# Performance work log

Hardware: AMD Instinct MI355X
Metric: run time of the kernel (lower is better)

The kernel has to match this reference:

```python
import jax, jax.numpy as jnp
import numpy as np

MAX_VISIT = 200
NUM_CODE = 506          # feature vocab -> 507 multi-hot dims
NUM_TGT = 284           # target vocab multi-hot dims
B = 64
P = 40                  # codes per visit
D_OTH = 57              # others feature dim (sign slice [37:] is 20-dim)
K = 100                 # len(weight_idx)
LSTM = 256
D_FEAT = (NUM_CODE + 1) + K + 27 + (D_OTH - 37)   # 654
D_FWD = D_FEAT + 10                                # 664
D_MLP_IN = (NUM_CODE + 1) + (D_OTH - 37) + 20 + 8  # 555


def multi_hot(codes, n):
    """Binary multi-hot encode int codes over last axis. codes: [..., P]."""
    shp = codes.shape
    flat = codes.reshape(-1, shp[-1])
    R = flat.shape[0]
    rows = jnp.repeat(jnp.arange(R), shp[-1])
    z = jnp.zeros((R, n), jnp.float32).at[rows, flat.reshape(-1)].set(1.0)
    return z.reshape(shp[:-1] + (n,))


def reverse_sequence(x, lengths):
    """tf.reverse_sequence along axis 1: reverse first lengths[i] steps, keep rest."""
    T = x.shape[1]
    j = jnp.arange(T)[None, :]
    L = lengths[:, None]
    idx = jnp.where(j < L, L - 1 - j, j)          # [B, T]
    return jnp.take_along_axis(x, idx[:, :, None], axis=1)


def setup_inputs() -> dict:
    key = jax.random.key(0)
    ks = jax.random.split(key, 13)
    code = jax.random.randint(ks[0], (B, MAX_VISIT, P), 0, NUM_CODE + 1, dtype=jnp.int32)
    others = jax.random.normal(ks[1], (B, MAX_VISIT, D_OTH), jnp.float32)
    length = jax.random.randint(ks[2], (B,), 3, MAX_VISIT + 1, dtype=jnp.int32)
    target = jax.random.randint(ks[3], (B, 10), 0, NUM_TGT, dtype=jnp.int32)
    weight_idx = jax.random.randint(ks[4], (K,), 0, NUM_TGT, dtype=jnp.int32)
    s = 0.02
    Wf = jax.random.normal(ks[5], (D_FWD, LSTM), jnp.float32) * s
    bf = jnp.zeros((LSTM,), jnp.float32)
    Wb = jax.random.normal(ks[6], (D_FWD, LSTM), jnp.float32) * s
    bb = jnp.zeros((LSTM,), jnp.float32)
    W0 = jax.random.normal(ks[7], (D_MLP_IN, 256), jnp.float32) * s
    b0 = jnp.zeros((256,), jnp.float32)
    W1 = jax.random.normal(ks[8], (256, 256), jnp.float32) * s
    b1 = jnp.zeros((256,), jnp.float32)
    return {"code": code, "others": others, "length": length, "target": target,
            "weight_idx": weight_idx, "Wf": Wf, "bf": bf, "Wb": Wb, "bb": bb,
            "W0": W0, "b0": b0, "W1": W1, "b1": b1}


def reference(code, others, length, target, weight_idx, Wf, bf, Wb, bb, W0, b0, W1, b1):
    code_mh = multi_hot(code, NUM_CODE + 1)                      # [B,200,507]
    # valid-visit mask (dense analogue of tf.boolean_mask over [B,198])
    mask = (jnp.arange(MAX_VISIT - 2)[None, :] < (length - 2)[:, None]).astype(jnp.float32)
    sign = others[:, 1:-1, 37:]                                  # [B,198,20]
    interval_ = jnp.concatenate([others[:, 1:-1, 27:37], others[:, 2:, 27:37]], axis=-1)
    stay = others[:, 1:-1, 19:27]
    x = jnp.concatenate([code_mh[:, 1:-1], sign, interval_, stay], axis=-1)  # [B,198,555]
    h = jax.nn.relu(x @ W0 + b0) @ W1 + b1                       # [B,198,256]
    fv = h / jnp.sqrt(jnp.sum(h * h, axis=-1, keepdims=True))
    fv = fv * mask[:, :, None]                                   # zero invalid rows
    # target block: gather (1 - multi-hot) at weight_idx, tile over visits
    tgt = 1.0 - multi_hot(target, NUM_TGT)                       # [B,284]
    tgt = tgt[:, weight_idx]                                     # [B,K]
    tgt = jnp.broadcast_to(tgt[:, None, :], (B, MAX_VISIT, K))
    code_full = jnp.concatenate([code_mh, tgt], axis=-1)         # [B,200,607]
    interval = others[:, :, 27:37]
    interval_backward = jnp.concatenate(
        [jnp.zeros((B, 1, 10), jnp.float32), reverse_sequence(interval, length)[:, :-1]], axis=1)
    feature = jnp.concatenate([code_full, others[:, :, :27], others[:, :, 37:]], axis=-1)
    feature_backward = reverse_sequence(feature, length)
    x_forward = jnp.concatenate([feature, interval], axis=-1)[:, :-2] @ Wf + bf
    x_backward = jnp.concatenate([feature_backward, interval_backward], axis=-1)[:, :-2] @ Wb + bb
    return (x_forward, x_backward, fv)
```

## Files before the change

### kernel.cpp

```cpp
#include <hip/hip_runtime.h>
#include <hip/hip_bf16.h>

typedef unsigned short u16;
typedef __attribute__((ext_vector_type(8))) short short8;
typedef __attribute__((ext_vector_type(4))) float f32x4;

#define TMAX 200
#define TOUT 198
#define PC 40
#define DOTH 57
#define NKT 9
#define FWD_OFF 0
#define BWD_OFF 3244032
#define FV_OFF  6488064
#define OWF 0
#define OWB 294912
#define OW0 589824
#define OW1 884736
#define OTF 1015808
#define OTB 1081344

__device__ __forceinline__ u16 f2b(float v) {
  __hip_bfloat16 h = __float2bfloat16(v);
  return *(u16*)&h;
}

__global__ __launch_bounds__(256) void prep_kernel(
    const int* __restrict__ target, const int* __restrict__ widx,
    const float* __restrict__ Wf, const float* __restrict__ bfv,
    const float* __restrict__ Wb, const float* __restrict__ bbv,
    const float* __restrict__ W0, const float* __restrict__ W1,
    u16* __restrict__ wsu, float* __restrict__ wsf)
{
  int blk = blockIdx.x, n = threadIdx.x;
  if (blk < 248) {
    const float* src; u16* dst; int kb; int mode;
    if (blk < 72)       { src=Wf; dst=wsu+OWF/2; kb=blk;     mode=0; }
    else if (blk < 144) { src=Wb; dst=wsu+OWB/2; kb=blk-72;  mode=0; }
    else if (blk < 216) { src=W0; dst=wsu+OW0/2; kb=blk-144; mode=1; }
    else                { src=W1; dst=wsu+OW1/2; kb=blk-216; mode=2; }
    u16 pk[8];
    #pragma unroll
    for (int j=0;j<8;j++) {
      int k = kb*8+j;
      int sr;
      if (mode==0)      sr = (k<57)? 607+k : (k<564)? k-57 : -1;
      else if (mode==1) sr = (k<48)? 507+k : (k<57)? -1 : (k<564)? k-57 : -1;
      else              sr = k;
      float v = (sr>=0)? src[sr*256+n] : 0.f;
      pk[j] = f2b(v);
    }
    *(uint4*)(dst + (kb*256+n)*8) = *(uint4*)pk;
  } else {
    int b = blk - 248;
    __shared__ float tval[100]; __shared__ int tg[10];
    if (n<10) tg[n]=target[b*10+n];
    __syncthreads();
    if (n<100){ int w=widx[n]; float v=1.f;
      #pragma unroll
      for(int i=0;i<10;i++) if(tg[i]==w) v=0.f;
      tval[n]=v; }
    __syncthreads();
    float aF=bfv[n], aB=bbv[n];
    for(int k=0;k<100;k++){ float v=tval[k];
      aF=fmaf(v,Wf[(507+k)*256+n],aF); aB=fmaf(v,Wb[(507+k)*256+n],aB); }
    wsf[OTF/4 + b*256+n]=aF; wsf[OTB/4 + b*256+n]=aB;
  }
}

__global__ __launch_bounds__(256) void gemm_kernel(
    const int* __restrict__ code, const float* __restrict__ others,
    const int* __restrict__ length,
    const float* __restrict__ b0, const float* __restrict__ b1,
    const u16* __restrict__ wsu, const float* __restrict__ wsf,
    float* __restrict__ out)
{
  const int tile = blockIdx.x;
  const int strm = blockIdx.y;
  const int tid = threadIdx.x;
  const int wv = tid>>6, lane = tid&63, q = lane>>4, c = lane&15;
  const int colbase = wv*64 + c;

  __shared__ u16 lA[3][2048];
  __shared__ int rowB[32], rowT[32], rowS[32], rowS2[32], rowL[32];
  __shared__ float rpart[4][32];

  if (tid < 32) {
    int m = tile*32 + tid;
    int b = m/198, t = m - b*198;
    int L = length[b];
    int s, s2 = 0;
    if (strm==0) s = t;
    else if (strm==1){ s = (t<L)? (L-1-t) : t;
                       s2 = (t==0)? -1 : (((t-1)<L)? (L-t) : (t-1)); }
    else s = t+1;
    rowB[tid]=b; rowT[tid]=t; rowS[tid]=s; rowS2[tid]=s2; rowL[tid]=L;
  }
  __syncthreads();

  int myp[5], myr[5];
  #pragma unroll
  for (int it=0; it<5; it++) {
    int idx = tid + it*256;
    int r = idx/40, p = idx - r*40;
    myr[it] = r*8;
    myp[it] = 57 + code[(rowB[r]*TMAX + rowS[r])*PC + p];
  }

  float dv[8];
  if (strm < 2) {
    #pragma unroll
    for (int it=0; it<8; it++) {
      int idx = tid + it*256;
      float v = 0.f;
      if (idx < 32*57) {
        int r = idx/57, j = idx - r*57;
        int col = (j<27)? j : (j<47)? 37+(j-27) : 27+(j-47);
        int sr = (strm==1 && j>=47)? rowS2[r] : rowS[r];
        if (sr >= 0) v = others[(rowB[r]*TMAX + sr)*DOTH + col];
      }
      dv[it] = v;
    }
  } else {
    #pragma unroll
    for (int it=0; it<6; it++) {
      int idx = tid + it*256;
      int r = idx/48, j = idx - r*48;
      int t = rowT[r], srow, col;
      if (j<20)      { srow=t+1; col=37+j; }
      else if (j<30) { srow=t+1; col=27+(j-20); }
      else if (j<40) { srow=t+2; col=27+(j-30); }
      else           { srow=t+1; col=19+(j-40); }
      dv[it] = others[(rowB[r]*TMAX + srow)*DOTH + col];
    }
  }

  f32x4 acc[2][4];
  if (strm < 2) {
    const float* tg = wsf + ((strm==0)? OTF/4 : OTB/4);
    #pragma unroll
    for (int mt=0; mt<2; mt++)
      #pragma unroll
      for (int reg=0; reg<4; reg++) {
        int rl = mt*16 + q*4 + reg;
        const float* tr = tg + rowB[rl]*256;
        #pragma unroll
        for (int nt=0; nt<4; nt++) acc[mt][nt][reg] = tr[colbase + nt*16];
      }
  } else {
    #pragma unroll
    for (int nt=0; nt<4; nt++){ float v = b0[colbase + nt*16];
      #pragma unroll
      for (int mt=0; mt<2; mt++)
        #pragma unroll
        for (int reg=0; reg<4; reg++) acc[mt][nt][reg]=v; }
  }

  { uint4 z = {0,0,0,0};
    ((uint4*)lA[0])[tid] = z; ((uint4*)lA[1])[tid] = z; }
  __syncthreads();
  #pragma unroll
  for (int it=0; it<5; it++) {
    unsigned d = (unsigned)(myp[it]);
    if (d < 64u) lA[0][(d>>3)*256 + myr[it] + (d&7)] = 0x3F80;
  }
  if (strm < 2) {
    #pragma unroll
    for (int it=0; it<8; it++) {
      int idx = tid + it*256;
      if (idx < 32*57) {
        int r = idx/57, j = idx - r*57;
        lA[0][(j>>3)*256 + r*8 + (j&7)] = f2b(dv[it]);
      }
    }
  } else {
    #pragma unroll
    for (int it=0; it<6; it++) {
      int idx = tid + it*256;
      int r = idx/48, j = idx - r*48;
      lA[0][(j>>3)*256 + r*8 + (j&7)] = f2b(dv[it]);
    }
  }
  __syncthreads();

  const u16* Wpk = wsu + ((strm==0)? OWF/2 : (strm==1)? OWB/2 : OW0/2);
  for (int kt=0; kt<NKT; kt++) {
    const u16* A = lA[kt%3];
    const u16* gB0 = Wpk + ((kt*8 + q    )*256 + colbase)*8;
    const u16* gB1 = Wpk + ((kt*8 + 4 + q)*256 + colbase)*8;
    short8 bf0[4], bf1[4];
    #pragma unroll
    for (int nt=0; nt<4; nt++) bf0[nt] = *(const short8*)(gB0 + nt*16*8);
    #pragma unroll
    for (int nt=0; nt<4; nt++) bf1[nt] = *(const short8*)(gB1 + nt*16*8);
    if (kt < 8) {
      u16* nb = lA[(kt+1)%3];
      const int k0n = (kt+1)*64;
      #pragma unroll
      for (int it=0; it<5; it++) {
        unsigned d = (unsigned)(myp[it] - k0n);
        if (d < 64u) nb[(d>>3)*256 + myr[it] + (d&7)] = 0x3F80;
      }
    }
    if (kt < 7) {
      uint4 z = {0,0,0,0};
      ((uint4*)lA[(kt+2)%3])[tid] = z;
    }
    short8 af0[2], af1[2];
    #pragma unroll
    for (int mt=0; mt<2; mt++) af0[mt] = *(const short8*)&A[(q    )*256 + (mt*16 + c)*8];
    #pragma unroll
    for (int mt=0; mt<2; mt++) af1[mt] = *(const short8*)&A[(4 + q)*256 + (mt*16 + c)*8];
    #pragma unroll
    for (int mt=0; mt<2; mt++)
      #pragma unroll
      for (int nt=0; nt<4; nt++)
        acc[mt][nt] = __builtin_amdgcn_mfma_f32_16x16x32_bf16(af0[mt], bf0[nt], acc[mt][nt], 0,0,0);
    #pragma unroll
    for (int mt=0; mt<2; mt++)
      #pragma unroll
      for (int nt=0; nt<4; nt++)
        acc[mt][nt] = __builtin_amdgcn_mfma_f32_16x16x32_bf16(af1[mt], bf1[nt], acc[mt][nt], 0,0,0);
    __syncthreads();
  }

  if (strm < 2) {
    float* o = out + ((strm==0)? FWD_OFF : BWD_OFF);
    #pragma unroll
    for (int mt=0; mt<2; mt++)
      #pragma unroll
      for (int reg=0; reg<4; reg++) {
        int rl = mt*16 + q*4 + reg;
        float* orow = o + (rowB[rl]*TOUT + rowT[rl])*256 + colbase;
        #pragma unroll
        for (int nt=0; nt<4; nt++) orow[nt*16] = acc[mt][nt][reg];
      }
  } else {
    if (wv == 0) {
      #pragma unroll
      for (int mt=0; mt<2; mt++)
        #pragma unroll
        for (int reg=0; reg<4; reg++) {
          int rl = mt*16 + q*4 + reg;
          #pragma unroll
          for (int nt=0; nt<4; nt++) {
            int kl = c + nt*16;
            lA[0][(kl>>3)*256 + rl*8 + (kl&7)] = f2b(fmaxf(acc[mt][nt][reg], 0.f));
          }
        }
    }
    __syncthreads();
    f32x4 a2[2][4];
    #pragma unroll
    for (int nt=0; nt<4; nt++){ float v = b1[colbase + nt*16];
      #pragma unroll
      for (int mt=0; mt<2; mt++)
        #pragma unroll
        for (int reg=0; reg<4; reg++) a2[mt][nt][reg]=v; }
    const u16* W1p = wsu + OW1/2;
    for (int kt2=0; kt2<4; kt2++) {
      if (wv == kt2+1) {
        u16* B2 = lA[(kt2+1)&1];
        #pragma unroll
        for (int mt=0; mt<2; mt++)
          #pragma unroll
          for (int reg=0; reg<4; reg++) {
            int rl = mt*16 + q*4 + reg;
            #pragma unroll
            for (int nt=0; nt<4; nt++) {
              int kl = c + nt*16;
              B2[(kl>>3)*256 + rl*8 + (kl&7)] = f2b(fmaxf(acc[mt][nt][reg], 0.f));
            }
          }
      }
      const u16* A2 = lA[kt2&1];
      #pragma unroll
      for (int s=0; s<2; s++) {
        int akb = s*4 + q;
        const u16* gB = W1p + ((kt2*8 + akb)*256 + colbase)*8;
        short8 af[2], bf[4];
        #pragma unroll
        for (int nt=0; nt<4; nt++) bf[nt] = *(const short8*)(gB + nt*16*8);
        #pragma unroll
        for (int mt=0; mt<2; mt++) af[mt] = *(const short8*)&A2[akb*256 + (mt*16 + c)*8];
        #pragma unroll
        for (int mt=0; mt<2; mt++)
          #pragma unroll
          for (int nt=0; nt<4; nt++)
            a2[mt][nt] = __builtin_amdgcn_mfma_f32_16x16x32_bf16(af[mt], bf[nt], a2[mt][nt], 0,0,0);
      }
      __syncthreads();
    }
    #pragma unroll
    for (int mt=0; mt<2; mt++)
      #pragma unroll
      for (int reg=0; reg<4; reg++) {
        int rl = mt*16 + q*4 + reg;
        float ss = 0.f;
        #pragma unroll
        for (int nt=0; nt<4; nt++){ float v=a2[mt][nt][reg]; ss = fmaf(v,v,ss); }
        ss += __shfl_xor(ss, 1, 64); ss += __shfl_xor(ss, 2, 64);
        ss += __shfl_xor(ss, 4, 64); ss += __shfl_xor(ss, 8, 64);
        if (c==0) rpart[wv][rl] = ss;
      }
    __syncthreads();
    #pragma unroll
    for (int mt=0; mt<2; mt++)
      #pragma unroll
      for (int reg=0; reg<4; reg++) {
        int rl = mt*16 + q*4 + reg;
        float s = rpart[0][rl]+rpart[1][rl]+rpart[2][rl]+rpart[3][rl];
        float inv = (s>0.f)? (1.0f/sqrtf(s)) : 0.f;
        int t = rowT[rl];
        if (t >= rowL[rl]-2) inv = 0.f;
        float* orow = out + FV_OFF + (rowB[rl]*TOUT + t)*256 + colbase;
        #pragma unroll
        for (int nt=0; nt<4; nt++) orow[nt*16] = a2[mt][nt][reg]*inv;
      }
  }
}

extern "C" void kernel_launch(void* const* d_in, const int* in_sizes, int n_in,
                              void* d_out, int out_size, void* d_ws, size_t ws_size,
                              hipStream_t stream) {
  const int*   code    = (const int*)d_in[0];
  const float* others  = (const float*)d_in[1];
  const int*   length  = (const int*)d_in[2];
  const int*   target  = (const int*)d_in[3];
  const int*   widx    = (const int*)d_in[4];
  const float* Wf      = (const float*)d_in[5];
  const float* bfv     = (const float*)d_in[6];
  const float* Wb      = (const float*)d_in[7];
  const float* bbv     = (const float*)d_in[8];
  const float* W0      = (const float*)d_in[9];
  const float* b0v     = (const float*)d_in[10];
  const float* W1      = (const float*)d_in[11];
  const float* b1v     = (const float*)d_in[12];

  u16*   wsu = (u16*)d_ws;
  float* wsf = (float*)d_ws;
  float* out = (float*)d_out;

  prep_kernel<<<dim3(312), dim3(256), 0, stream>>>(target, widx, Wf, bfv, Wb, bbv, W0, W1, wsu, wsf);
  gemm_kernel<<<dim3(396,3), dim3(256), 0, stream>>>(code, others, length,
      b0v, b1v, wsu, wsf, out);
}
```

Before: 122.3 us.

## Prefetch weight tiles one step ahead and skip fully masked MLP tiles

The GEMM k-loops now double-buffer the B-operand (weight) fragments in registers, so the next k-step's global loads are issued before the current MFMAs run, and both loops are fully unrolled. In the MLP stream, a tile whose rows all fall beyond the valid length (masked to zero in the output) now writes zeros and exits early instead of computing the MLP. This hides global weight-load latency and avoids wasted work, at the cost of more registers, which could reduce occupancy.

After: 121.4 us. No clear change (-0.7%).

```diff
diff --git a/kernel.cpp b/kernel.cpp
--- a/kernel.cpp
+++ b/kernel.cpp
@@ -84,7 +84,9 @@
   __shared__ u16 lA[3][2048];
   __shared__ int rowB[32], rowT[32], rowS[32], rowS2[32], rowL[32];
   __shared__ float rpart[4][32];
-
+  __shared__ int s_skip;
+
+  if (tid == 0) s_skip = 1;
   if (tid < 32) {
     int m = tile*32 + tid;
     int b = m/198, t = m - b*198;
@@ -98,6 +100,21 @@
   }
   __syncthreads();
 
+  if (strm == 2) {
+    if (tid < 32 && rowT[tid] < rowL[tid]-2) s_skip = 0;
+    __syncthreads();
+    if (s_skip) {
+      f32x4 z = {0.f, 0.f, 0.f, 0.f};
+      #pragma unroll
+      for (int it=0; it<8; it++) {
+        int lin = it*256 + tid;
+        int r = lin>>6, c4 = (lin&63)<<2;
+        *(f32x4*)(out + FV_OFF + (rowB[r]*TOUT + rowT[r])*256 + c4) = z;
+      }
+      return;
+    }
+  }
+
   int myp[5], myr[5];
   #pragma unroll
   for (int it=0; it<5; it++) {
@@ -156,6 +173,18 @@
         for (int reg=0; reg<4; reg++) acc[mt][nt][reg]=v; }
   }
 
+  const u16* Wpk = wsu + ((strm==0)? OWF/2 : (strm==1)? OWB/2 : OW0/2);
+  short8 bb[2][8];
+  {
+    const u16* gB0 = Wpk + ((q    )*256 + colbase)*8;
+    const u16* gB1 = Wpk + ((4 + q)*256 + colbase)*8;
+    #pragma unroll
+    for (int nt=0; nt<4; nt++) {
+      bb[0][nt]   = *(const short8*)(gB0 + nt*128);
+      bb[0][nt+4] = *(const short8*)(gB1 + nt*128);
+    }
+  }
+
   { uint4 z = {0,0,0,0};
     ((uint4*)lA[0])[tid] = z; ((uint4*)lA[1])[tid] = z; }
   __syncthreads();
@@ -183,17 +212,24 @@
   }
   __syncthreads();
 
-  const u16* Wpk = wsu + ((strm==0)? OWF/2 : (strm==1)? OWB/2 : OW0/2);
+  #pragma unroll
   for (int kt=0; kt<NKT; kt++) {
     const u16* A = lA[kt%3];
-    const u16* gB0 = Wpk + ((kt*8 + q    )*256 + colbase)*8;
-    const u16* gB1 = Wpk + ((kt*8 + 4 + q)*256 + colbase)*8;
-    short8 bf0[4], bf1[4];
-    #pragma unroll
-    for (int nt=0; nt<4; nt++) bf0[nt] = *(const short8*)(gB0 + nt*16*8);
-    #pragma unroll
-    for (int nt=0; nt<4; nt++) bf1[nt] = *(const short8*)(gB1 + nt*16*8);
-    if (kt < 8) {
+    short8 af0[2], af1[2];
+    #pragma unroll
+    for (int mt=0; mt<2; mt++) af0[mt] = *(const short8*)&A[(q    )*256 + (mt*16 + c)*8];
+    #pragma unroll
+    for (int mt=0; mt<2; mt++) af1[mt] = *(const short8*)&A[(4 + q)*256 + (mt*16 + c)*8];
+    if (kt < NKT-1) {
+      const u16* gB0 = Wpk + (((kt+1)*8 + q    )*256 + colbase)*8;
+      const u16* gB1 = Wpk + (((kt+1)*8 + 4 + q)*256 + colbase)*8;
+      #pragma unroll
+      for (int nt=0; nt<4; nt++) {
+        bb[(kt+1)&1][nt]   = *(const short8*)(gB0 + nt*128);
+        bb[(kt+1)&1][nt+4] = *(const short8*)(gB1 + nt*128);
+      }
+    }
+    if (kt < NKT-1) {
       u16* nb = lA[(kt+1)%3];
       const int k0n = (kt+1)*64;
       #pragma unroll
@@ -202,25 +238,20 @@
         if (d < 64u) nb[(d>>3)*256 + myr[it] + (d&7)] = 0x3F80;
       }
     }
-    if (kt < 7) {
+    if (kt < NKT-2) {
       uint4 z = {0,0,0,0};
       ((uint4*)lA[(kt+2)%3])[tid] = z;
     }
-    short8 af0[2], af1[2];
-    #pragma unroll
-    for (int mt=0; mt<2; mt++) af0[mt] = *(const short8*)&A[(q    )*256 + (mt*16 + c)*8];
-    #pragma unroll
-    for (int mt=0; mt<2; mt++) af1[mt] = *(const short8*)&A[(4 + q)*256 + (mt*16 + c)*8];
     #pragma unroll
     for (int mt=0; mt<2; mt++)
       #pragma unroll
       for (int nt=0; nt<4; nt++)
-        acc[mt][nt] = __builtin_amdgcn_mfma_f32_16x16x32_bf16(af0[mt], bf0[nt], acc[mt][nt], 0,0,0);
+        acc[mt][nt] = __builtin_amdgcn_mfma_f32_16x16x32_bf16(af0[mt], bb[kt&1][nt], acc[mt][nt], 0,0,0);
     #pragma unroll
     for (int mt=0; mt<2; mt++)
       #pragma unroll
       for (int nt=0; nt<4; nt++)
-        acc[mt][nt] = __builtin_amdgcn_mfma_f32_16x16x32_bf16(af1[mt], bf1[nt], acc[mt][nt], 0,0,0);
+        acc[mt][nt] = __builtin_amdgcn_mfma_f32_16x16x32_bf16(af1[mt], bb[kt&1][nt+4], acc[mt][nt], 0,0,0);
     __syncthreads();
   }
 
@@ -249,6 +280,13 @@
           }
         }
     }
+    const u16* W1p = wsu + OW1/2;
+    short8 bw[2][4];
+    {
+      const u16* gB = W1p + ((q)*256 + colbase)*8;
+      #pragma unroll
+      for (int nt=0; nt<4; nt++) bw[0][nt] = *(const short8*)(gB + nt*128);
+    }
     __syncthreads();
     f32x4 a2[2][4];
     #pragma unroll
@@ -257,7 +295,7 @@
       for (int mt=0; mt<2; mt++)
         #pragma unroll
         for (int reg=0; reg<4; reg++) a2[mt][nt][reg]=v; }
-    const u16* W1p = wsu + OW1/2;
+    #pragma unroll
     for (int kt2=0; kt2<4; kt2++) {
       if (wv == kt2+1) {
         u16* B2 = lA[(kt2+1)&1];
@@ -273,21 +311,25 @@
             }
           }
       }
-      const u16* A2 = lA[kt2&1];
       #pragma unroll
       for (int s=0; s<2; s++) {
+        const int step = kt2*2 + s;
+        const u16* A2 = lA[kt2&1];
         int akb = s*4 + q;
-        const u16* gB = W1p + ((kt2*8 + akb)*256 + colbase)*8;
-        short8 af[2], bf[4];
-        #pragma unroll
-        for (int nt=0; nt<4; nt++) bf[nt] = *(const short8*)(gB + nt*16*8);
+        short8 af[2];
         #pragma unroll
         for (int mt=0; mt<2; mt++) af[mt] = *(const short8*)&A2[akb*256 + (mt*16 + c)*8];
+        if (step < 7) {
+          const int nstep = step + 1;
+          const u16* gB = W1p + (((nstep>>1)*8 + (nstep&1)*4 + q)*256 + colbase)*8;
+          #pragma unroll
+          for (int nt=0; nt<4; nt++) bw[nstep&1][nt] = *(const short8*)(gB + nt*128);
+        }
         #pragma unroll
         for (int mt=0; mt<2; mt++)
           #pragma unroll
           for (int nt=0; nt<4; nt++)
-            a2[mt][nt] = __builtin_amdgcn_mfma_f32_16x16x32_bf16(af[mt], bf[nt], a2[mt][nt], 0,0,0);
+            a2[mt][nt] = __builtin_amdgcn_mfma_f32_16x16x32_bf16(af[mt], bw[step&1][nt], a2[mt][nt], 0,0,0);
       }
       __syncthreads();
     }
```
